# Kernel tuning notes

Measured on AMD Instinct MI355X. Metric: run time of the kernel, lower is better.

## Reference

```python
import jax, jax.numpy as jnp
import numpy as np

MASK_NUM = -2.0**32 + 1.0  # additive masking constant from the original layer


def setup_inputs() -> dict:
    key = jax.random.key(0)
    k1, k2, k3, k4 = jax.random.split(key, 4)
    BH, S, D = 32, 2048, 64  # batch*heads, seq_len, head_dim
    B = 4                    # original batch (masks are per-batch, tiled by heads)
    queries = jax.random.normal(k1, (BH, S, D), dtype=jnp.float32)
    keys_ = jax.random.normal(k2, (BH, S, D), dtype=jnp.float32)
    values = jax.random.normal(k3, (BH, S, D), dtype=jnp.float32)
    masks = jax.random.randint(k4, (B, S), 0, 2, dtype=jnp.int32)
    return {"queries": queries, "keys": keys_, "values": values, "masks": masks}


def reference(queries, keys, values, masks):
    BH, S, D = queries.shape
    # scores = Q K^T / sqrt(D)   -> [BH, S, S]
    scores = jnp.einsum("bqd,bkd->bqk", queries, keys) / (D ** 0.5)
    # key-padding mask: masks [B, S] tiled along axis 0 by BH // B, broadcast over query dim
    reps = BH // masks.shape[0]
    m = jnp.tile(masks.astype(jnp.float32), (reps, 1))[:, None, :]  # [BH, 1, S]
    scores = scores + m * MASK_NUM
    # causal (future) mask: keep lower triangle, replace rest with MASK_NUM
    tril = jnp.tril(jnp.ones((S, S), dtype=jnp.float32))
    scores = jnp.where(tril == 0, jnp.float32(MASK_NUM), scores)
    attn = jax.nn.softmax(scores, axis=-1)
    # dropout_rate = 0.0 -> identity
    return jnp.einsum("bqk,bkd->bqd", attn, values)
```

## Files before the change

kernel.cpp:

```cpp
#include <hip/hip_runtime.h>
#include <stdint.h>

#define S_LEN 2048
#define HDIM  64
#define NHEAD 32
#define NBATCH 4
#define QK_SCALE (0.125f * 1.44269504088896341f)
#define DEFER_THR 8.0f
#define NEG_BIG (-1e30f)

typedef float f32x4 __attribute__((ext_vector_type(4)));
typedef short bf16x8 __attribute__((ext_vector_type(8)));

#define WS_MB    0
#define WS_MVP   1024
#define WS_KBF   132096
#define KVB      (NHEAD * 32 * 8192)
#define WS_VTBF  (WS_KBF + (size_t)KVB)

static __device__ __forceinline__ unsigned int cvt_pk_bf16(float lo, float hi) {
    unsigned int r;
    asm("v_cvt_pk_bf16_f32 %0, %1, %2" : "=v"(r) : "v"(lo), "v"(hi));
    return r;
}
static __device__ __forceinline__ float bf2f(unsigned short u) {
    return __uint_as_float((unsigned int)u << 16);
}
static __device__ __forceinline__ void load_lds16(const void* g, void* l) {
    __builtin_amdgcn_global_load_lds(
        (const __attribute__((address_space(1))) uint32_t*)g,
        (__attribute__((address_space(3))) uint32_t*)l, 16, 0, 0);
}

__global__ __launch_bounds__(256) void cvt_kernel(
    const float* __restrict__ K, const float* __restrict__ V,
    const int* __restrict__ masks,
    uint8_t* __restrict__ Kbf, uint8_t* __restrict__ Vtbf,
    unsigned short* __restrict__ mvp, unsigned long long* __restrict__ MB)
{
    const int bid = blockIdx.x;
    const int xcd = bid & 7, rem = bid >> 3;
    const int bh  = xcd * 4 + (rem >> 5);
    const int t   = rem & 31;
    const int tid = threadIdx.x, lane = tid & 63, w = tid >> 6;
    const size_t ho  = (size_t)bh * S_LEN * HDIM;
    const size_t img = ((size_t)bh * 32 + t) * 8192;

    {
        const int kr = tid >> 2;
        const int kc = (tid & 3) << 4;
        const float4* kp = (const float4*)(K + ho + (size_t)(t * 64 + kr) * HDIM + kc);
        float4 a0 = kp[0], a1 = kp[1], a2 = kp[2], a3 = kp[3];
        int4 kv0, kv1;
        kv0.x = cvt_pk_bf16(a0.x, a0.y); kv0.y = cvt_pk_bf16(a0.z, a0.w);
        kv0.z = cvt_pk_bf16(a1.x, a1.y); kv0.w = cvt_pk_bf16(a1.z, a1.w);
        kv1.x = cvt_pk_bf16(a2.x, a2.y); kv1.y = cvt_pk_bf16(a2.z, a2.w);
        kv1.z = cvt_pk_bf16(a3.x, a3.y); kv1.w = cvt_pk_bf16(a3.z, a3.w);
        const int swz = (kr & 7) << 4;
        *(int4*)&Kbf[img + ((kr * 128 + kc * 2)      ^ swz)] = kv0;
        *(int4*)&Kbf[img + ((kr * 128 + kc * 2 + 16) ^ swz)] = kv1;
    }
    {
        const int vd = lane;
        const int vk = w * 16;
        const float* vp = V + ho + (size_t)(t * 64 + vk) * HDIM + vd;
        float va[16];
        float psum = 0.f;
        #pragma unroll
        for (int i = 0; i < 16; ++i) { va[i] = vp[(size_t)i * HDIM]; psum += va[i]; }
        int4 vv0, vv1;
        vv0.x = cvt_pk_bf16(va[0],  va[1]);  vv0.y = cvt_pk_bf16(va[2],  va[3]);
        vv0.z = cvt_pk_bf16(va[4],  va[5]);  vv0.w = cvt_pk_bf16(va[6],  va[7]);
        vv1.x = cvt_pk_bf16(va[8],  va[9]);  vv1.y = cvt_pk_bf16(va[10], va[11]);
        vv1.z = cvt_pk_bf16(va[12], va[13]); vv1.w = cvt_pk_bf16(va[14], va[15]);
        const int swz = (vd & 7) << 4;
        *(int4*)&Vtbf[img + ((vd * 128 + vk * 2)      ^ swz)] = vv0;
        *(int4*)&Vtbf[img + ((vd * 128 + vk * 2 + 16) ^ swz)] = vv1;
        __shared__ float red[4][64];
        red[w][vd] = psum;
        __syncthreads();
        if (tid < 64) {
            float tot = red[0][tid] + red[1][tid] + red[2][tid] + red[3][tid];
            mvp[(bh * 32 + t) * 64 + tid] = (unsigned short)(cvt_pk_bf16(tot * (1.0f / (float)S_LEN), 0.f) & 0xFFFF);
        }
    }
    if (bh < NBATCH && tid < 64) {
        const int m = masks[bh * S_LEN + t * 64 + lane];
        const unsigned long long bits = __ballot(m != 0);
        if (lane == 0) MB[bh * 32 + t] = bits;
    }
}

__global__ __launch_bounds__(256) void attn_fwd(
    const float* __restrict__ Q,
    const unsigned short* __restrict__ mvp,
    const unsigned long long* __restrict__ MB,
    const uint8_t* __restrict__ Kbf, const uint8_t* __restrict__ Vtbf,
    float* __restrict__ out)
{
    extern __shared__ __align__(16) char lds[];
    const int tid  = threadIdx.x;
    const int lane = tid & 63;
    const int w    = tid >> 6;
    const int lq   = lane & 15;
    const int lk   = lane >> 4;

    const int bid  = blockIdx.x;
    const int nbid = (bid & 7) * 64 + (bid >> 3);
    const int bh   = nbid >> 4;
    const int j    = nbid & 15;
    const int b    = bh & (NBATCH - 1);

    const size_t ho = (size_t)bh * S_LEN * HDIM;
    const float* Qh = Q + ho;
    const uint8_t* kimg = Kbf  + (size_t)bh * 32 * 8192;
    const uint8_t* vimg = Vtbf + (size_t)bh * 32 * 8192;

    auto STAGE = [&](int img0, bool two, int bufb) {
        const uint8_t* gk = kimg + (size_t)img0 * 8192 + w * 2048 + lane * 16;
        const uint8_t* gv = vimg + (size_t)img0 * 8192 + w * 2048 + lane * 16;
        char* lk0 = &lds[bufb + w * 2048];
        char* lv0 = &lds[bufb + 16384 + w * 2048];
        load_lds16(gk,        lk0);
        load_lds16(gk + 1024, lk0 + 1024);
        load_lds16(gv,        lv0);
        load_lds16(gv + 1024, lv0 + 1024);
        if (two) {
            load_lds16(gk + 8192, lk0 + 8192);
            load_lds16(gk + 9216, lk0 + 9216);
            load_lds16(gv + 8192, lv0 + 8192);
            load_lds16(gv + 9216, lv0 + 9216);
        }
    };

    const int swz   = (lq & 7) << 4;
    const int pswz  = (lq & 15) << 4;
    const int pbase = 65536 + (w << 12);
    const int prow  = lq << 8;

    #pragma unroll 1
    for (int pass = 0; pass < 2; ++pass) {
        const int qb = pass ? (31 - j) : j;
        const int q0 = qb * 64;
        const int nt = (qb >> 1) + 1;
        const int wqa = q0 + w * 16 + lq;

        bf16x8 qf[2];
        {
            const float* qrow = Qh + (size_t)(q0 + w * 16 + lq) * HDIM;
            #pragma unroll
            for (int c = 0; c < 2; ++c) {
                const int d0 = lk * 8 + c * 32;
                float4 f0 = *(const float4*)(qrow + d0);
                float4 f1 = *(const float4*)(qrow + d0 + 4);
                int4 qi;
                qi.x = cvt_pk_bf16(f0.x * QK_SCALE, f0.y * QK_SCALE);
                qi.y = cvt_pk_bf16(f0.z * QK_SCALE, f0.w * QK_SCALE);
                qi.z = cvt_pk_bf16(f1.x * QK_SCALE, f1.y * QK_SCALE);
                qi.w = cvt_pk_bf16(f1.z * QK_SCALE, f1.w * QK_SCALE);
                qf[c] = *(bf16x8*)&qi;
            }
        }

        f32x4 acc[4];
        #pragma unroll
        for (int g = 0; g < 4; ++g) acc[g] = (f32x4){0.f, 0.f, 0.f, 0.f};
        float m_r = 0.f;
        float l_r = 0.f;

        STAGE(0, qb >= 1, 0);
        __syncthreads();

        for (int it = 0; it < nt; ++it) {
            const int kb     = (it & 1) << 15;
            const bool diag  = (it == nt - 1);
            const bool skipHi = diag && ((qb & 1) == 0);
            if (!diag) {
                const int a = 2 * it + 2;
                STAGE(a, (a + 1) <= qb, kb ^ 32768);
            }

            f32x4 sacc[8];
            #pragma unroll
            for (int g = 0; g < 8; ++g) sacc[g] = (f32x4){0.f, 0.f, 0.f, 0.f};
            __builtin_amdgcn_s_setprio(1);
            #pragma unroll
            for (int c = 0; c < 2; ++c) {
                #pragma unroll
                for (int g = 0; g < 4; ++g) {
                    bf16x8 kf = *(const bf16x8*)&lds[kb + ((16 * g + lq) * 128 + ((16 * lk + 64 * c) ^ swz))];
                    sacc[g] = __builtin_amdgcn_mfma_f32_16x16x32_bf16(kf, qf[c], sacc[g], 0, 0, 0);
                }
            }
            if (!skipHi) {
                #pragma unroll
                for (int c = 0; c < 2; ++c) {
                    #pragma unroll
                    for (int g = 4; g < 8; ++g) {
                        bf16x8 kf = *(const bf16x8*)&lds[kb + 8192 + ((16 * (g - 4) + lq) * 128 + ((16 * lk + 64 * c) ^ swz))];
                        sacc[g] = __builtin_amdgcn_mfma_f32_16x16x32_bf16(kf, qf[c], sacc[g], 0, 0, 0);
                    }
                }
            }
            __builtin_amdgcn_s_setprio(0);

            if (diag) {
                const int wqrel = wqa - it * 128;
                #pragma unroll
                for (int g = 0; g < 8; ++g)
                    #pragma unroll
                    for (int r = 0; r < 4; ++r)
                        if (16 * g + 4 * lk + r > wqrel) sacc[g][r] = NEG_BIG;
            }
            const unsigned long long mb0 = MB[(b << 5) + 2 * it];
            const unsigned long long mb1 = MB[(b << 5) + 2 * it + 1];
            float mloc = NEG_BIG;
            #pragma unroll
            for (int g = 0; g < 8; ++g) {
                const unsigned long long mbw = (g < 4) ? mb0 : mb1;
                const unsigned int nib = (unsigned int)(mbw >> (16 * (g & 3) + 4 * lk)) & 0xFu;
                #pragma unroll
                for (int r = 0; r < 4; ++r) {
                    float s = ((nib >> r) & 1u) ? NEG_BIG : sacc[g][r];
                    sacc[g][r] = s;
                    mloc = fmaxf(mloc, s);
                }
            }
            mloc = fmaxf(mloc, __shfl_xor(mloc, 16, 64));
            mloc = fmaxf(mloc, __shfl_xor(mloc, 32, 64));

            if (!__all(mloc - m_r <= DEFER_THR)) {
                const float newm = fmaxf(m_r, mloc);
                const float sc = exp2f(m_r - newm);
                l_r *= sc;
                m_r = newm;
                float scb[4];
                #pragma unroll
                for (int r = 0; r < 4; ++r) scb[r] = __shfl(sc, 4 * lk + r, 64);
                #pragma unroll
                for (int g = 0; g < 4; ++g)
                    #pragma unroll
                    for (int r = 0; r < 4; ++r) acc[g][r] *= scb[r];
            }

            float ls0 = 0.f, ls1 = 0.f;
            #pragma unroll
            for (int g = 0; g < 8; ++g) {
                #pragma unroll
                for (int r = 0; r < 4; ++r) {
                    float e = exp2f(sacc[g][r] - m_r);
                    sacc[g][r] = e;
                    if (g & 1) ls1 += e; else ls0 += e;
                }
            }
            float ls = ls0 + ls1;
            ls += __shfl_xor(ls, 16, 64);
            ls += __shfl_xor(ls, 32, 64);
            l_r += ls;

            #pragma unroll
            for (int g = 0; g < 4; ++g) {
                uint2 pw;
                pw.x = cvt_pk_bf16(sacc[g][0], sacc[g][1]);
                pw.y = cvt_pk_bf16(sacc[g][2], sacc[g][3]);
                *(uint2*)&lds[pbase + prow + (((32 * g + 8 * lk)) ^ pswz)] = pw;
            }
            if (!skipHi) {
                #pragma unroll
                for (int g = 4; g < 8; ++g) {
                    uint2 pw;
                    pw.x = cvt_pk_bf16(sacc[g][0], sacc[g][1]);
                    pw.y = cvt_pk_bf16(sacc[g][2], sacc[g][3]);
                    *(uint2*)&lds[pbase + prow + (((32 * g + 8 * lk)) ^ pswz)] = pw;
                }
            }

            __builtin_amdgcn_s_setprio(1);
            #pragma unroll
            for (int c = 0; c < 2; ++c) {
                bf16x8 pa = *(const bf16x8*)&lds[pbase + prow + ((64 * c + 16 * lk) ^ pswz)];
                #pragma unroll
                for (int g = 0; g < 4; ++g) {
                    bf16x8 vb = *(const bf16x8*)&lds[kb + 16384 + ((lq + 16 * g) * 128 + ((16 * lk + 64 * c) ^ swz))];
                    acc[g] = __builtin_amdgcn_mfma_f32_16x16x32_bf16(pa, vb, acc[g], 0, 0, 0);
                }
            }
            if (!skipHi) {
                #pragma unroll
                for (int c = 2; c < 4; ++c) {
                    bf16x8 pa = *(const bf16x8*)&lds[pbase + prow + ((64 * c + 16 * lk) ^ pswz)];
                    #pragma unroll
                    for (int g = 0; g < 4; ++g) {
                        bf16x8 vb = *(const bf16x8*)&lds[kb + 16384 + 8192 + ((lq + 16 * g) * 128 + ((16 * lk + 64 * (c - 2)) ^ swz))];
                        acc[g] = __builtin_amdgcn_mfma_f32_16x16x32_bf16(pa, vb, acc[g], 0, 0, 0);
                    }
                }
            }
            __builtin_amdgcn_s_setprio(0);

            __syncthreads();
        }

        float lr_b[4];
        #pragma unroll
        for (int r = 0; r < 4; ++r) lr_b[r] = __shfl(l_r, 4 * lk + r, 64);
        #pragma unroll
        for (int r = 0; r < 4; ++r) {
            const int qrow = q0 + w * 16 + 4 * lk + r;
            float* orow = out + ho + (size_t)qrow * HDIM;
            if (lr_b[r] == 0.f) {
                #pragma unroll
                for (int g = 0; g < 4; ++g) {
                    float s = 0.f;
                    for (int tt = 0; tt < 32; ++tt)
                        s += bf2f(mvp[(bh * 32 + tt) * 64 + lq + 16 * g]);
                    orow[lq + 16 * g] = s;
                }
            } else {
                const float inv = 1.0f / lr_b[r];
                #pragma unroll
                for (int g = 0; g < 4; ++g) orow[lq + 16 * g] = acc[g][r] * inv;
            }
        }
    }
}

extern "C" void kernel_launch(void* const* d_in, const int* in_sizes, int n_in,
                              void* d_out, int out_size, void* d_ws, size_t ws_size,
                              hipStream_t stream)
{
    const float* Q     = (const float*)d_in[0];
    const float* K     = (const float*)d_in[1];
    const float* V     = (const float*)d_in[2];
    const int*   masks = (const int*)d_in[3];
    float* out = (float*)d_out;

    char* ws = (char*)d_ws;
    unsigned long long* MB = (unsigned long long*)(ws + WS_MB);
    unsigned short* mvp    = (unsigned short*)(ws + WS_MVP);
    uint8_t* Kbf  = (uint8_t*)(ws + WS_KBF);
    uint8_t* Vtbf = (uint8_t*)(ws + WS_VTBF);

    hipFuncSetAttribute(reinterpret_cast<const void*>(&attn_fwd),
                        hipFuncAttributeMaxDynamicSharedMemorySize, 81920);

    cvt_kernel<<<dim3(1024), dim3(256), 0, stream>>>(K, V, masks, Kbf, Vtbf, mvp, MB);
    attn_fwd<<<dim3(512), dim3(256), 81920, stream>>>(Q, mvp, MB, Kbf, Vtbf, out);
}
```

Before: 145.8 us.

## Rewrite attention with 32x32 MFMA tiles, register-resident P, 128-key blocks

```diff
diff --git a/kernel.cpp b/kernel.cpp
--- a/kernel.cpp
+++ b/kernel.cpp
@@ -9,19 +9,22 @@
 #define DEFER_THR 8.0f
 #define NEG_BIG (-1e30f)
 
-typedef float f32x4 __attribute__((ext_vector_type(4)));
+typedef float f32x16 __attribute__((ext_vector_type(16)));
 typedef short bf16x8 __attribute__((ext_vector_type(8)));
 
-#define WS_MB    0
-#define WS_MVP   1024
-#define WS_KBF   132096
-#define KVB      (NHEAD * 32 * 8192)
-#define WS_VTBF  (WS_KBF + (size_t)KVB)
+#define WS_MB   0
+#define WS_MVP  1024
+#define WS_KBF  66560
+#define IMGB    (NHEAD * 16 * 16384)
+#define WS_VTBF (WS_KBF + (size_t)IMGB)
 
 static __device__ __forceinline__ unsigned int cvt_pk_bf16(float lo, float hi) {
     unsigned int r;
     asm("v_cvt_pk_bf16_f32 %0, %1, %2" : "=v"(r) : "v"(lo), "v"(hi));
     return r;
+}
+static __device__ __forceinline__ void permswap(unsigned int& a, unsigned int& b) {
+    asm("v_permlane32_swap_b32 %0, %1" : "+v"(a), "+v"(b));
 }
 static __device__ __forceinline__ float bf2f(unsigned short u) {
     return __uint_as_float((unsigned int)u << 16);
@@ -39,59 +42,66 @@
     unsigned short* __restrict__ mvp, unsigned long long* __restrict__ MB)
 {
     const int bid = blockIdx.x;
-    const int xcd = bid & 7, rem = bid >> 3;
-    const int bh  = xcd * 4 + (rem >> 5);
-    const int t   = rem & 31;
-    const int tid = threadIdx.x, lane = tid & 63, w = tid >> 6;
+    const int bh  = (bid & 7) * 4 + ((bid >> 3) >> 4);
+    const int t   = (bid >> 3) & 15;
+    const int tid = threadIdx.x;
     const size_t ho  = (size_t)bh * S_LEN * HDIM;
-    const size_t img = ((size_t)bh * 32 + t) * 8192;
+    const size_t img = ((size_t)bh * 16 + t) * 16384;
 
     {
-        const int kr = tid >> 2;
-        const int kc = (tid & 3) << 4;
-        const float4* kp = (const float4*)(K + ho + (size_t)(t * 64 + kr) * HDIM + kc);
-        float4 a0 = kp[0], a1 = kp[1], a2 = kp[2], a3 = kp[3];
-        int4 kv0, kv1;
-        kv0.x = cvt_pk_bf16(a0.x, a0.y); kv0.y = cvt_pk_bf16(a0.z, a0.w);
-        kv0.z = cvt_pk_bf16(a1.x, a1.y); kv0.w = cvt_pk_bf16(a1.z, a1.w);
-        kv1.x = cvt_pk_bf16(a2.x, a2.y); kv1.y = cvt_pk_bf16(a2.z, a2.w);
-        kv1.z = cvt_pk_bf16(a3.x, a3.y); kv1.w = cvt_pk_bf16(a3.z, a3.w);
-        const int swz = (kr & 7) << 4;
-        *(int4*)&Kbf[img + ((kr * 128 + kc * 2)      ^ swz)] = kv0;
-        *(int4*)&Kbf[img + ((kr * 128 + kc * 2 + 16) ^ swz)] = kv1;
+        const int kr = tid >> 1;
+        const int dh = (tid & 1) * 32;
+        const float4* kp = (const float4*)(K + ho + (size_t)(t * 128 + kr) * HDIM + dh);
+        float4 a[8];
+        #pragma unroll
+        for (int i = 0; i < 8; ++i) a[i] = kp[i];
+        const int rowb = (kr & 63) * 256 + (kr >> 6) * 128;
+        const int swz  = (kr & 7) << 4;
+        #pragma unroll
+        for (int ci = 0; ci < 4; ++ci) {
+            int4 wv;
+            wv.x = cvt_pk_bf16(a[2*ci].x,   a[2*ci].y);
+            wv.y = cvt_pk_bf16(a[2*ci].z,   a[2*ci].w);
+            wv.z = cvt_pk_bf16(a[2*ci+1].x, a[2*ci+1].y);
+            wv.w = cvt_pk_bf16(a[2*ci+1].z, a[2*ci+1].w);
+            *(int4*)&Kbf[img + rowb + ((dh * 2 + 16 * ci) ^ swz)] = wv;
+        }
     }
     {
-        const int vd = lane;
-        const int vk = w * 16;
-        const float* vp = V + ho + (size_t)(t * 64 + vk) * HDIM + vd;
-        float va[16];
+        const int d  = tid & 63;
+        const int kg = tid >> 6;
+        const float* vp = V + ho + (size_t)(t * 128 + kg * 32) * HDIM + d;
+        float va[32];
         float psum = 0.f;
         #pragma unroll
-        for (int i = 0; i < 16; ++i) { va[i] = vp[(size_t)i * HDIM]; psum += va[i]; }
-        int4 vv0, vv1;
-        vv0.x = cvt_pk_bf16(va[0],  va[1]);  vv0.y = cvt_pk_bf16(va[2],  va[3]);
-        vv0.z = cvt_pk_bf16(va[4],  va[5]);  vv0.w = cvt_pk_bf16(va[6],  va[7]);
-        vv1.x = cvt_pk_bf16(va[8],  va[9]);  vv1.y = cvt_pk_bf16(va[10], va[11]);
-        vv1.z = cvt_pk_bf16(va[12], va[13]); vv1.w = cvt_pk_bf16(va[14], va[15]);
-        const int swz = (vd & 7) << 4;
-        *(int4*)&Vtbf[img + ((vd * 128 + vk * 2)      ^ swz)] = vv0;
-        *(int4*)&Vtbf[img + ((vd * 128 + vk * 2 + 16) ^ swz)] = vv1;
+        for (int i = 0; i < 32; ++i) { va[i] = vp[(size_t)i * HDIM]; psum += va[i]; }
+        const int swz = (d & 15) << 4;
+        #pragma unroll
+        for (int ci = 0; ci < 4; ++ci) {
+            int4 wv;
+            wv.x = cvt_pk_bf16(va[8*ci+0], va[8*ci+1]);
+            wv.y = cvt_pk_bf16(va[8*ci+2], va[8*ci+3]);
+            wv.z = cvt_pk_bf16(va[8*ci+4], va[8*ci+5]);
+            wv.w = cvt_pk_bf16(va[8*ci+6], va[8*ci+7]);
+            *(int4*)&Vtbf[img + d * 256 + ((kg * 64 + 16 * ci) ^ swz)] = wv;
+        }
         __shared__ float red[4][64];
-        red[w][vd] = psum;
+        red[kg][d] = psum;
         __syncthreads();
         if (tid < 64) {
             float tot = red[0][tid] + red[1][tid] + red[2][tid] + red[3][tid];
-            mvp[(bh * 32 + t) * 64 + tid] = (unsigned short)(cvt_pk_bf16(tot * (1.0f / (float)S_LEN), 0.f) & 0xFFFF);
-        }
-    }
-    if (bh < NBATCH && tid < 64) {
-        const int m = masks[bh * S_LEN + t * 64 + lane];
+            mvp[(bh * 16 + t) * 64 + tid] =
+                (unsigned short)(cvt_pk_bf16(tot * (1.0f / (float)S_LEN), 0.f) & 0xFFFF);
+        }
+    }
+    if (bh < NBATCH && tid < 128) {
+        const int m = masks[bh * S_LEN + t * 128 + tid];
         const unsigned long long bits = __ballot(m != 0);
-        if (lane == 0) MB[bh * 32 + t] = bits;
-    }
-}
-
-__global__ __launch_bounds__(256) void attn_fwd(
+        if ((tid & 63) == 0) MB[bh * 32 + t * 2 + (tid >> 6)] = bits;
+    }
+}
+
+__global__ __launch_bounds__(256, 2) void attn_fwd(
     const float* __restrict__ Q,
     const unsigned short* __restrict__ mvp,
     const unsigned long long* __restrict__ MB,
@@ -102,225 +112,197 @@
     const int tid  = threadIdx.x;
     const int lane = tid & 63;
     const int w    = tid >> 6;
-    const int lq   = lane & 15;
-    const int lk   = lane >> 4;
-
-    const int bid  = blockIdx.x;
-    const int nbid = (bid & 7) * 64 + (bid >> 3);
-    const int bh   = nbid >> 4;
-    const int j    = nbid & 15;
-    const int b    = bh & (NBATCH - 1);
+    const int h    = lane >> 5;
+    const int l31  = lane & 31;
+    const int swzK7  = (lane & 7)  << 4;
+    const int swzV15 = (lane & 15) << 4;
+
+    const int bid = blockIdx.x;
+    const int r   = bid >> 3;
+    const int bh  = (bid & 7) * 4 + (r >> 4);
+    const int tt  = r & 15;
+    const int qb  = (tt & 1) ? (tt >> 1) : (15 - (tt >> 1));
+    const int b   = bh & (NBATCH - 1);
+    const int q0  = qb * 128;
+    const int nt  = qb + 1;
+    const int wq  = q0 + w * 32 + l31;
 
     const size_t ho = (size_t)bh * S_LEN * HDIM;
-    const float* Qh = Q + ho;
-    const uint8_t* kimg = Kbf  + (size_t)bh * 32 * 8192;
-    const uint8_t* vimg = Vtbf + (size_t)bh * 32 * 8192;
-
-    auto STAGE = [&](int img0, bool two, int bufb) {
-        const uint8_t* gk = kimg + (size_t)img0 * 8192 + w * 2048 + lane * 16;
-        const uint8_t* gv = vimg + (size_t)img0 * 8192 + w * 2048 + lane * 16;
-        char* lk0 = &lds[bufb + w * 2048];
-        char* lv0 = &lds[bufb + 16384 + w * 2048];
-        load_lds16(gk,        lk0);
-        load_lds16(gk + 1024, lk0 + 1024);
-        load_lds16(gv,        lv0);
-        load_lds16(gv + 1024, lv0 + 1024);
-        if (two) {
-            load_lds16(gk + 8192, lk0 + 8192);
-            load_lds16(gk + 9216, lk0 + 9216);
-            load_lds16(gv + 8192, lv0 + 8192);
-            load_lds16(gv + 9216, lv0 + 9216);
+    const uint8_t* kimg = Kbf  + (size_t)bh * 16 * 16384;
+    const uint8_t* vimg = Vtbf + (size_t)bh * 16 * 16384;
+
+    auto STAGE = [&](int ti, int bufb) {
+        const uint8_t* gk = kimg + (size_t)ti * 16384 + tid * 16;
+        const uint8_t* gv = vimg + (size_t)ti * 16384 + tid * 16;
+        char* dk = &lds[bufb + tid * 16];
+        char* dv = &lds[bufb + 16384 + tid * 16];
+        #pragma unroll
+        for (int c = 0; c < 4; ++c) {
+            load_lds16(gk + c * 4096, dk + c * 4096);
+            load_lds16(gv + c * 4096, dv + c * 4096);
         }
     };
 
-    const int swz   = (lq & 7) << 4;
-    const int pswz  = (lq & 15) << 4;
-    const int pbase = 65536 + (w << 12);
-    const int prow  = lq << 8;
-
-    #pragma unroll 1
-    for (int pass = 0; pass < 2; ++pass) {
-        const int qb = pass ? (31 - j) : j;
-        const int q0 = qb * 64;
-        const int nt = (qb >> 1) + 1;
-        const int wqa = q0 + w * 16 + lq;
-
-        bf16x8 qf[2];
-        {
-            const float* qrow = Qh + (size_t)(q0 + w * 16 + lq) * HDIM;
-            #pragma unroll
-            for (int c = 0; c < 2; ++c) {
-                const int d0 = lk * 8 + c * 32;
-                float4 f0 = *(const float4*)(qrow + d0);
-                float4 f1 = *(const float4*)(qrow + d0 + 4);
-                int4 qi;
-                qi.x = cvt_pk_bf16(f0.x * QK_SCALE, f0.y * QK_SCALE);
-                qi.y = cvt_pk_bf16(f0.z * QK_SCALE, f0.w * QK_SCALE);
-                qi.z = cvt_pk_bf16(f1.x * QK_SCALE, f1.y * QK_SCALE);
-                qi.w = cvt_pk_bf16(f1.z * QK_SCALE, f1.w * QK_SCALE);
-                qf[c] = *(bf16x8*)&qi;
-            }
-        }
-
-        f32x4 acc[4];
-        #pragma unroll
-        for (int g = 0; g < 4; ++g) acc[g] = (f32x4){0.f, 0.f, 0.f, 0.f};
-        float m_r = 0.f;
-        float l_r = 0.f;
-
-        STAGE(0, qb >= 1, 0);
+    bf16x8 qf[4];
+    {
+        const float* qrow = Q + ho + (size_t)wq * HDIM;
+        #pragma unroll
+        for (int c = 0; c < 4; ++c) {
+            const int d0 = 16 * c + 8 * h;
+            float4 f0 = *(const float4*)(qrow + d0);
+            float4 f1 = *(const float4*)(qrow + d0 + 4);
+            int4 qi;
+            qi.x = cvt_pk_bf16(f0.x * QK_SCALE, f0.y * QK_SCALE);
+            qi.y = cvt_pk_bf16(f0.z * QK_SCALE, f0.w * QK_SCALE);
+            qi.z = cvt_pk_bf16(f1.x * QK_SCALE, f1.y * QK_SCALE);
+            qi.w = cvt_pk_bf16(f1.z * QK_SCALE, f1.w * QK_SCALE);
+            qf[c] = *(bf16x8*)&qi;
+        }
+    }
+
+    f32x16 acc[2];
+    #pragma unroll
+    for (int i = 0; i < 16; ++i) { acc[0][i] = 0.f; acc[1][i] = 0.f; }
+    float m_r = 0.f;
+    float l_r = 0.f;
+
+    STAGE(0, 0);
+    __syncthreads();
+
+    for (int it = 0; it < nt; ++it) {
+        const int kb = (it & 1) << 15;
+        if (it + 1 < nt) STAGE(it + 1, kb ^ 32768);
+
+        f32x16 s[4];
+        #pragma unroll
+        for (int g = 0; g < 4; ++g)
+            #pragma unroll
+            for (int i = 0; i < 16; ++i) s[g][i] = 0.f;
+        __builtin_amdgcn_s_setprio(1);
+        #pragma unroll
+        for (int g = 0; g < 4; ++g) {
+            const int rowb = kb + (l31 + 32 * (g & 1)) * 256 + (g >> 1) * 128;
+            #pragma unroll
+            for (int c = 0; c < 4; ++c) {
+                bf16x8 kf = *(const bf16x8*)&lds[rowb + ((32 * c + 16 * h) ^ swzK7)];
+                s[g] = __builtin_amdgcn_mfma_f32_32x32x16_bf16(kf, qf[c], s[g], 0, 0, 0);
+            }
+        }
+        __builtin_amdgcn_s_setprio(0);
+
+        unsigned long long mb0 = MB[(b << 5) + 2 * it];
+        unsigned long long mb1 = MB[(b << 5) + 2 * it + 1];
+        if (it == nt - 1) {
+            const int wr = wq & 127;
+            mb0 |= (wr >= 63) ? 0ull : (~0ull << (wr + 1));
+            const int r1 = wr - 64;
+            mb1 |= (r1 >= 63) ? 0ull : ((r1 < 0) ? ~0ull : (~0ull << (r1 + 1)));
+        }
+        const unsigned long long w0 = mb0 >> (4 * h), w1 = mb1 >> (4 * h);
+        const unsigned int wgs[4] = { (unsigned int)w0, (unsigned int)(w0 >> 32),
+                                      (unsigned int)w1, (unsigned int)(w1 >> 32) };
+
+        float mloc = NEG_BIG;
+        #pragma unroll
+        for (int g = 0; g < 4; ++g) {
+            const unsigned int wg = wgs[g];
+            #pragma unroll
+            for (int i = 0; i < 16; ++i) {
+                const int c = (i & 3) + 8 * (i >> 2);
+                float v = ((wg >> c) & 1u) ? NEG_BIG : s[g][i];
+                s[g][i] = v;
+                mloc = fmaxf(mloc, v);
+            }
+        }
+        mloc = fmaxf(mloc, __shfl_xor(mloc, 32, 64));
+
+        if (!__all(mloc - m_r <= DEFER_THR)) {
+            const float newm = fmaxf(m_r, mloc);
+            const float sc = exp2f(m_r - newm);
+            l_r *= sc; m_r = newm;
+            #pragma unroll
+            for (int i = 0; i < 16; ++i) {
+                const float sci = __shfl(sc, (i & 3) + 8 * (i >> 2) + 4 * h, 64);
+                acc[0][i] *= sci; acc[1][i] *= sci;
+            }
+        }
+
+        bf16x8 pf[8];
+        float lsg[4];
+        #pragma unroll
+        for (int g = 0; g < 4; ++g) {
+            float p[16];
+            #pragma unroll
+            for (int i = 0; i < 16; ++i) p[i] = exp2f(s[g][i] - m_r);
+            float a0 = (p[0] + p[1]) + (p[2] + p[3]);
+            float a1 = (p[4] + p[5]) + (p[6] + p[7]);
+            float a2 = (p[8] + p[9]) + (p[10] + p[11]);
+            float a3 = (p[12] + p[13]) + (p[14] + p[15]);
+            lsg[g] = (a0 + a1) + (a2 + a3);
+            unsigned int Ap[4], Bp[4];
+            #pragma unroll
+            for (int s4 = 0; s4 < 4; ++s4) {
+                Ap[s4] = cvt_pk_bf16(p[4*s4+0], p[4*s4+1]);
+                Bp[s4] = cvt_pk_bf16(p[4*s4+2], p[4*s4+3]);
+            }
+            {
+                unsigned int r0 = Ap[0], r2 = Ap[1]; permswap(r0, r2);
+                unsigned int r1 = Bp[0], r3 = Bp[1]; permswap(r1, r3);
+                int4 f = { (int)r0, (int)r1, (int)r2, (int)r3 };
+                pf[2*g] = *(bf16x8*)&f;
+            }
+            {
+                unsigned int r0 = Ap[2], r2 = Ap[3]; permswap(r0, r2);
+                unsigned int r1 = Bp[2], r3 = Bp[3]; permswap(r1, r3);
+                int4 f = { (int)r0, (int)r1, (int)r2, (int)r3 };
+                pf[2*g+1] = *(bf16x8*)&f;
+            }
+        }
+        float ls = (lsg[0] + lsg[1]) + (lsg[2] + lsg[3]);
+        ls += __shfl_xor(ls, 32, 64);
+        l_r += ls;
+
+        __builtin_amdgcn_s_setprio(1);
+        #pragma unroll
+        for (int kp = 0; kp < 8; ++kp) {
+            #pragma unroll
+            for (int nd = 0; nd < 2; ++nd) {
+                bf16x8 vf = *(const bf16x8*)&lds[kb + 16384 + (32 * nd + l31) * 256
+                                                + ((32 * kp + 16 * h) ^ swzV15)];
+                acc[nd] = __builtin_amdgcn_mfma_f32_32x32x16_bf16(pf[kp], vf, acc[nd], 0, 0, 0);
+            }
+        }
+        __builtin_amdgcn_s_setprio(0);
+
         __syncthreads();
-
-        for (int it = 0; it < nt; ++it) {
-            const int kb     = (it & 1) << 15;
-            const bool diag  = (it == nt - 1);
-            const bool skipHi = diag && ((qb & 1) == 0);
-            if (!diag) {
-                const int a = 2 * it + 2;
-                STAGE(a, (a + 1) <= qb, kb ^ 32768);
-            }
-
-            f32x4 sacc[8];
-            #pragma unroll
-            for (int g = 0; g < 8; ++g) sacc[g] = (f32x4){0.f, 0.f, 0.f, 0.f};
-            __builtin_amdgcn_s_setprio(1);
-            #pragma unroll
-            for (int c = 0; c < 2; ++c) {
-                #pragma unroll
-                for (int g = 0; g < 4; ++g) {
-                    bf16x8 kf = *(const bf16x8*)&lds[kb + ((16 * g + lq) * 128 + ((16 * lk + 64 * c) ^ swz))];
-                    sacc[g] = __builtin_amdgcn_mfma_f32_16x16x32_bf16(kf, qf[c], sacc[g], 0, 0, 0);
-                }
-            }
-            if (!skipHi) {
-                #pragma unroll
-                for (int c = 0; c < 2; ++c) {
-                    #pragma unroll
-                    for (int g = 4; g < 8; ++g) {
-                        bf16x8 kf = *(const bf16x8*)&lds[kb + 8192 + ((16 * (g - 4) + lq) * 128 + ((16 * lk + 64 * c) ^ swz))];
-                        sacc[g] = __builtin_amdgcn_mfma_f32_16x16x32_bf16(kf, qf[c], sacc[g], 0, 0, 0);
-                    }
-                }
-            }
-            __builtin_amdgcn_s_setprio(0);
-
-            if (diag) {
-                const int wqrel = wqa - it * 128;
-                #pragma unroll
-                for (int g = 0; g < 8; ++g)
-                    #pragma unroll
-                    for (int r = 0; r < 4; ++r)
-                        if (16 * g + 4 * lk + r > wqrel) sacc[g][r] = NEG_BIG;
-            }
-            const unsigned long long mb0 = MB[(b << 5) + 2 * it];
-            const unsigned long long mb1 = MB[(b << 5) + 2 * it + 1];
-            float mloc = NEG_BIG;
-            #pragma unroll
-            for (int g = 0; g < 8; ++g) {
-                const unsigned long long mbw = (g < 4) ? mb0 : mb1;
-                const unsigned int nib = (unsigned int)(mbw >> (16 * (g & 3) + 4 * lk)) & 0xFu;
-                #pragma unroll
-                for (int r = 0; r < 4; ++r) {
-                    float s = ((nib >> r) & 1u) ? NEG_BIG : sacc[g][r];
-                    sacc[g][r] = s;
-                    mloc = fmaxf(mloc, s);
-                }
-            }
-            mloc = fmaxf(mloc, __shfl_xor(mloc, 16, 64));
-            mloc = fmaxf(mloc, __shfl_xor(mloc, 32, 64));
-
-            if (!__all(mloc - m_r <= DEFER_THR)) {
-                const float newm = fmaxf(m_r, mloc);
-                const float sc = exp2f(m_r - newm);
-                l_r *= sc;
-                m_r = newm;
-                float scb[4];
-                #pragma unroll
-                for (int r = 0; r < 4; ++r) scb[r] = __shfl(sc, 4 * lk + r, 64);
-                #pragma unroll
-                for (int g = 0; g < 4; ++g)
-                    #pragma unroll
-                    for (int r = 0; r < 4; ++r) acc[g][r] *= scb[r];
-            }
-
-            float ls0 = 0.f, ls1 = 0.f;
-            #pragma unroll
-            for (int g = 0; g < 8; ++g) {
-                #pragma unroll
-                for (int r = 0; r < 4; ++r) {
-                    float e = exp2f(sacc[g][r] - m_r);
-                    sacc[g][r] = e;
-                    if (g & 1) ls1 += e; else ls0 += e;
-                }
-            }
-            float ls = ls0 + ls1;
-            ls += __shfl_xor(ls, 16, 64);
-            ls += __shfl_xor(ls, 32, 64);
-            l_r += ls;
-
-            #pragma unroll
-            for (int g = 0; g < 4; ++g) {
-                uint2 pw;
-                pw.x = cvt_pk_bf16(sacc[g][0], sacc[g][1]);
-                pw.y = cvt_pk_bf16(sacc[g][2], sacc[g][3]);
-                *(uint2*)&lds[pbase + prow + (((32 * g + 8 * lk)) ^ pswz)] = pw;
-            }
-            if (!skipHi) {
-                #pragma unroll
-                for (int g = 4; g < 8; ++g) {
-                    uint2 pw;
-                    pw.x = cvt_pk_bf16(sacc[g][0], sacc[g][1]);
-                    pw.y = cvt_pk_bf16(sacc[g][2], sacc[g][3]);
-                    *(uint2*)&lds[pbase + prow + (((32 * g + 8 * lk)) ^ pswz)] = pw;
-                }
-            }
-
-            __builtin_amdgcn_s_setprio(1);
-            #pragma unroll
-            for (int c = 0; c < 2; ++c) {
-                bf16x8 pa = *(const bf16x8*)&lds[pbase + prow + ((64 * c + 16 * lk) ^ pswz)];
-                #pragma unroll
-                for (int g = 0; g < 4; ++g) {
-                    bf16x8 vb = *(const bf16x8*)&lds[kb + 16384 + ((lq + 16 * g) * 128 + ((16 * lk + 64 * c) ^ swz))];
-                    acc[g] = __builtin_amdgcn_mfma_f32_16x16x32_bf16(pa, vb, acc[g], 0, 0, 0);
-                }
-            }
-            if (!skipHi) {
-                #pragma unroll
-                for (int c = 2; c < 4; ++c) {
-                    bf16x8 pa = *(const bf16x8*)&lds[pbase + prow + ((64 * c + 16 * lk) ^ pswz)];
-                    #pragma unroll
-                    for (int g = 0; g < 4; ++g) {
-                        bf16x8 vb = *(const bf16x8*)&lds[kb + 16384 + 8192 + ((lq + 16 * g) * 128 + ((16 * lk + 64 * (c - 2)) ^ swz))];
-                        acc[g] = __builtin_amdgcn_mfma_f32_16x16x32_bf16(pa, vb, acc[g], 0, 0, 0);
-                    }
-                }
-            }
-            __builtin_amdgcn_s_setprio(0);
-
-            __syncthreads();
-        }
-
-        float lr_b[4];
-        #pragma unroll
-        for (int r = 0; r < 4; ++r) lr_b[r] = __shfl(l_r, 4 * lk + r, 64);
-        #pragma unroll
-        for (int r = 0; r < 4; ++r) {
-            const int qrow = q0 + w * 16 + 4 * lk + r;
-            float* orow = out + ho + (size_t)qrow * HDIM;
-            if (lr_b[r] == 0.f) {
-                #pragma unroll
-                for (int g = 0; g < 4; ++g) {
-                    float s = 0.f;
-                    for (int tt = 0; tt < 32; ++tt)
-                        s += bf2f(mvp[(bh * 32 + tt) * 64 + lq + 16 * g]);
-                    orow[lq + 16 * g] = s;
-                }
-            } else {
-                const float inv = 1.0f / lr_b[r];
-                #pragma unroll
-                for (int g = 0; g < 4; ++g) orow[lq + 16 * g] = acc[g][r] * inv;
-            }
+    }
+
+    float lrv[16];
+    bool deadl = false;
+    #pragma unroll
+    for (int i = 0; i < 16; ++i) {
+        lrv[i] = __shfl(l_r, (i & 3) + 8 * (i >> 2) + 4 * h, 64);
+        deadl |= (lrv[i] == 0.f);
+    }
+    float mv0 = 0.f, mv1 = 0.f;
+    if (__any(deadl)) {
+        #pragma unroll
+        for (int ttn = 0; ttn < 16; ++ttn) {
+            mv0 += bf2f(mvp[(bh * 16 + ttn) * 64 + l31]);
+            mv1 += bf2f(mvp[(bh * 16 + ttn) * 64 + l31 + 32]);
+        }
+    }
+    #pragma unroll
+    for (int i = 0; i < 16; ++i) {
+        const int qrow = q0 + w * 32 + (i & 3) + 8 * (i >> 2) + 4 * h;
+        float* o = out + ho + (size_t)qrow * HDIM + l31;
+        if (lrv[i] == 0.f) {
+            o[0]  = mv0;
+            o[32] = mv1;
+        } else {
+            const float inv = 1.0f / lrv[i];
+            o[0]  = acc[0][i] * inv;
+            o[32] = acc[1][i] * inv;
         }
     }
 }
@@ -342,8 +324,8 @@
     uint8_t* Vtbf = (uint8_t*)(ws + WS_VTBF);
 
     hipFuncSetAttribute(reinterpret_cast<const void*>(&attn_fwd),
-                        hipFuncAttributeMaxDynamicSharedMemorySize, 81920);
-
-    cvt_kernel<<<dim3(1024), dim3(256), 0, stream>>>(K, V, masks, Kbf, Vtbf, mvp, MB);
-    attn_fwd<<<dim3(512), dim3(256), 81920, stream>>>(Q, mvp, MB, Kbf, Vtbf, out);
-}
+                        hipFuncAttributeMaxDynamicSharedMemorySize, 65536);
+
+    cvt_kernel<<<dim3(512), dim3(256), 0, stream>>>(K, V, masks, Kbf, Vtbf, mvp, MB);
+    attn_fwd<<<dim3(512), dim3(256), 65536, stream>>>(Q, mvp, MB, Kbf, Vtbf, out);
+}
```

Result: slower. 165.9 us (+13.8%).
